# Kernel optimization log

Measured on AMD Instinct MI355X. Metric: run time of the kernel, lower is better.

## Reference

```python
import jax, jax.numpy as jnp
import numpy as np

B, L, G, H = 16384, 4096, 30000, 256
LN_EPS = 1e-5


def setup_inputs() -> dict:
    key = jax.random.key(0)
    k0, k1, k2, k3 = jax.random.split(key, 4)
    x = jax.random.uniform(k0, (B, L), dtype=jnp.float32)          # cell x gene expression
    gene_idx = jax.random.randint(k1, (L,), 0, G)                   # irregular gene indices
    emb = jax.random.normal(k2, (G, H), dtype=jnp.float32) * 0.005  # gene embedding table
    W1 = jax.random.normal(k3, (H, H), dtype=jnp.float32) * (1.0 / np.sqrt(H))
    b1 = jnp.zeros((H,), dtype=jnp.float32)
    gamma = jnp.ones((H,), dtype=jnp.float32)
    beta = jnp.zeros((H,), dtype=jnp.float32)
    return {"x": x, "emb": emb, "W1": W1, "b1": b1, "gamma": gamma,
            "beta": beta, "gene_idx": gene_idx}


def reference(x, emb, W1, b1, gamma, beta, gene_idx):
    # OmicsEmbedder: gather gene embeddings, then weighted aggregation per cell
    feat = emb[gene_idx]                     # [L, H]  F.embedding gather
    h = x @ feat                             # [B, H]  torch.sparse.mm(x, feat)
    # extra_linear: Linear -> ReLU -> Dropout(eval: identity) -> LayerNorm
    h = jax.nn.relu(h @ W1 + b1)             # [B, H]
    mu = jnp.mean(h, axis=-1, keepdims=True)
    var = jnp.mean(jnp.square(h - mu), axis=-1, keepdims=True)
    return gamma * (h - mu) * jax.lax.rsqrt(var + LN_EPS) + beta
```

## Files before the change

### kernel.cpp

```cpp
#include <hip/hip_runtime.h>
#include <stdint.h>

#define B_DIM 16384
#define L_DIM 4096
#define H_DIM 256
#define LN_EPS 1e-5f

typedef unsigned short u16;
typedef __attribute__((ext_vector_type(4))) float f32x4;
typedef __attribute__((ext_vector_type(8))) short short8;

__device__ __forceinline__ u16 f2bf(float f) {
  union { float f; uint32_t u; } v; v.f = f;
  uint32_t u = v.u;
  u += 0x7FFFu + ((u >> 16) & 1u);
  return (u16)(u >> 16);
}

__device__ __forceinline__ short8 cvt8(const float4& u, const float4& v) {
  short8 o;
  o[0] = (short)f2bf(u.x); o[1] = (short)f2bf(u.y);
  o[2] = (short)f2bf(u.z); o[3] = (short)f2bf(u.w);
  o[4] = (short)f2bf(v.x); o[5] = (short)f2bf(v.y);
  o[6] = (short)f2bf(v.z); o[7] = (short)f2bf(v.w);
  return o;
}

__device__ __forceinline__ void gload_lds16(const void* g, void* l) {
  __builtin_amdgcn_global_load_lds((const __attribute__((address_space(1))) void*)g,
                                   (__attribute__((address_space(3))) void*)l, 16, 0, 0);
}

__global__ __launch_bounds__(256) void prep_frag(const float* __restrict__ src,
                                                 const int* __restrict__ idx,
                                                 u16* __restrict__ dst) {
  const int t = threadIdx.x;
  const int l = t & 63;
  const int w = t >> 6;
  const int frag = blockIdx.x * 4 + w;
  const int kstep = frag >> 4;
  const int nt = frag & 15;
  const int n = nt * 16 + (l & 15);
  const int kbase = kstep * 32 + (l >> 4) * 8;
  short8 v;
#pragma unroll
  for (int j = 0; j < 8; ++j) {
    const int k = kbase + j;
    const int g = idx ? idx[k] : k;
    v[j] = (short)f2bf(src[(size_t)g * H_DIM + n]);
  }
  *reinterpret_cast<short8*>(dst + ((size_t)frag * 64 + l) * 8) = v;
}

__global__ __launch_bounds__(256, 2) void fused(const float* __restrict__ x,
                                                const u16* __restrict__ fragB,
                                                const u16* __restrict__ fragW,
                                                const float* __restrict__ b1,
                                                const float* __restrict__ gmm,
                                                const float* __restrict__ bta,
                                                float* __restrict__ out) {
  __shared__ __align__(16) char pool[73728];
  const int t = threadIdx.x;
  const int l = t & 63;
  const int wv = t >> 6;
  const int m0 = blockIdx.x * 32;
  char* const Ab = pool + 65536;

  const int sr = t >> 3;
  const int sc = t & 7;
  const float* xsrc = x + (size_t)(m0 + sr) * L_DIM + sc * 8;
  const int awoff = sr * 128 + ((sc ^ (sr & 7)) << 4);

  float4 aP0 = *(const float4*)(xsrc);
  float4 aP1 = *(const float4*)(xsrc + 4);
#pragma unroll
  for (int i = 0; i < 8; ++i) {
    const int j = wv * 8 + i;
    gload_lds16(fragB + (size_t)((j >> 4) * 16 + (j & 15)) * 512 + l * 8,
                pool + j * 1024);
  }
  float4 aQ0 = *(const float4*)(xsrc + 64);
  float4 aQ1 = *(const float4*)(xsrc + 68);
  asm volatile("s_waitcnt vmcnt(0)" ::: "memory");
  *(short8*)(Ab + awoff) = cvt8(aP0, aP1);
  asm volatile("s_waitcnt lgkmcnt(0)" ::: "memory");
  __builtin_amdgcn_s_barrier();

  f32x4 acc[2][4] = {};

  auto stage = [&](int S, const float4& WR0, const float4& WR1,
                   float4& LD0, float4& LD1) {
    asm volatile("s_waitcnt vmcnt(0)" ::: "memory");
    __builtin_amdgcn_s_barrier();
    __builtin_amdgcn_sched_barrier(0);
    if (S < 63) {
      const u16* srcB = fragB + (size_t)(2 * (S + 1)) * 16 * 512;
      char* dstB = pool + ((S + 1) & 1) * 32768;
#pragma unroll
      for (int i = 0; i < 8; ++i) {
        const int j = wv * 8 + i;
        gload_lds16(srcB + (size_t)((j >> 4) * 16 + (j & 15)) * 512 + l * 8,
                    dstB + j * 1024);
      }
    }
    __builtin_amdgcn_sched_barrier(0);
    if (S < 63)
      *(short8*)(Ab + ((S + 1) & 1) * 4096 + awoff) = cvt8(WR0, WR1);
    if (S < 62) {
      const float* xn = xsrc + (S + 2) * 64;
      LD0 = *(const float4*)(xn);
      LD1 = *(const float4*)(xn + 4);
    }
    __builtin_amdgcn_sched_barrier(0);
    const char* bB = pool + (S & 1) * 32768;
    const char* bA = Ab + (S & 1) * 4096;
#pragma unroll
    for (int ks = 0; ks < 2; ++ks) {
      short8 af[2];
#pragma unroll
      for (int mi = 0; mi < 2; ++mi)
        af[mi] = *(const short8*)(bA + (mi * 16 + (l & 15)) * 128 +
                                  (((ks * 4 + (l >> 4)) ^ (l & 7)) << 4));
#pragma unroll
      for (int ntl = 0; ntl < 4; ++ntl) {
        const short8 bfv = *(const short8*)(bB + (ks * 16 + wv * 4 + ntl) * 1024 + l * 16);
#pragma unroll
        for (int mi = 0; mi < 2; ++mi)
          acc[mi][ntl] = __builtin_amdgcn_mfma_f32_16x16x32_bf16(af[mi], bfv, acc[mi][ntl], 0, 0, 0);
      }
    }
    asm volatile("s_waitcnt lgkmcnt(0)" ::: "memory");
    __builtin_amdgcn_s_barrier();
  };

  for (int sp = 0; sp < 32; ++sp) {
    stage(sp * 2,     aQ0, aQ1, aP0, aP1);
    stage(sp * 2 + 1, aP0, aP1, aQ0, aQ1);
  }

#pragma unroll
  for (int i = 0; i < 4; ++i) {
    const int j = wv * 4 + i;
    gload_lds16(fragW + (size_t)j * 512 + l * 8, pool + 16384 + j * 1024);
  }
#pragma unroll
  for (int mi = 0; mi < 2; ++mi)
#pragma unroll
    for (int rr = 0; rr < 4; ++rr) {
      const int row = mi * 16 + (l >> 4) * 4 + rr;
#pragma unroll
      for (int ntl = 0; ntl < 4; ++ntl) {
        const int col = wv * 64 + ntl * 16 + (l & 15);
        const int ls = (col >> 3) ^ (row & 15);
        *(u16*)(pool + row * 512 + ls * 16 + (col & 7) * 2) = f2bf(acc[mi][ntl][rr]);
      }
    }
  asm volatile("s_waitcnt lgkmcnt(0)" ::: "memory");
  __builtin_amdgcn_s_barrier();

  f32x4 acc2[2][4] = {};
  for (int kt = 0; kt < 8; ++kt) {
    asm volatile("s_waitcnt vmcnt(0)" ::: "memory");
    __builtin_amdgcn_s_barrier();
    __builtin_amdgcn_sched_barrier(0);
    if (kt < 7) {
      const u16* srcW = fragW + (size_t)(kt + 1) * 16 * 512;
      char* dstW = pool + 16384 + ((kt + 1) & 1) * 16384;
#pragma unroll
      for (int i = 0; i < 4; ++i) {
        const int j = wv * 4 + i;
        gload_lds16(srcW + (size_t)j * 512 + l * 8, dstW + j * 1024);
      }
    }
    __builtin_amdgcn_sched_barrier(0);
    const char* bW = pool + 16384 + (kt & 1) * 16384;
    short8 af[2];
#pragma unroll
    for (int mi = 0; mi < 2; ++mi) {
      const int row = mi * 16 + (l & 15);
      af[mi] = *(const short8*)(pool + row * 512 +
                                (((kt * 4 + (l >> 4)) ^ (row & 15)) << 4));
    }
#pragma unroll
    for (int ntl = 0; ntl < 4; ++ntl) {
      const short8 bfv = *(const short8*)(bW + (wv * 4 + ntl) * 1024 + l * 16);
#pragma unroll
      for (int mi = 0; mi < 2; ++mi)
        acc2[mi][ntl] = __builtin_amdgcn_mfma_f32_16x16x32_bf16(af[mi], bfv, acc2[mi][ntl], 0, 0, 0);
    }
    asm volatile("s_waitcnt lgkmcnt(0)" ::: "memory");
    __builtin_amdgcn_s_barrier();
  }

  float bv[4], gg[4], bb[4];
#pragma unroll
  for (int ntl = 0; ntl < 4; ++ntl) {
    const int col = wv * 64 + ntl * 16 + (l & 15);
    bv[ntl] = b1[col]; gg[ntl] = gmm[col]; bb[ntl] = bta[col];
  }
  float* lnred = (float*)(pool + 49152);
#pragma unroll
  for (int mi = 0; mi < 2; ++mi)
#pragma unroll
    for (int rr = 0; rr < 4; ++rr) {
      float s = 0.f, q = 0.f;
#pragma unroll
      for (int ntl = 0; ntl < 4; ++ntl) {
        const float v = fmaxf(acc2[mi][ntl][rr] + bv[ntl], 0.f);
        acc2[mi][ntl][rr] = v; s += v; q += v * v;
      }
#pragma unroll
      for (int m = 1; m < 16; m <<= 1) { s += __shfl_xor(s, m); q += __shfl_xor(q, m); }
      if ((l & 15) == 0) {
        const int row = mi * 16 + (l >> 4) * 4 + rr;
        lnred[(wv * 32 + row) * 2 + 0] = s;
        lnred[(wv * 32 + row) * 2 + 1] = q;
      }
    }
  __syncthreads();
#pragma unroll
  for (int mi = 0; mi < 2; ++mi)
#pragma unroll
    for (int rr = 0; rr < 4; ++rr) {
      const int row = mi * 16 + (l >> 4) * 4 + rr;
      float S = 0.f, Q = 0.f;
#pragma unroll
      for (int w2 = 0; w2 < 4; ++w2) {
        S += lnred[(w2 * 32 + row) * 2 + 0];
        Q += lnred[(w2 * 32 + row) * 2 + 1];
      }
      const float mu = S * (1.0f / 256.0f);
      const float rstd = rsqrtf(Q * (1.0f / 256.0f) - mu * mu + LN_EPS);
      float* op = out + (size_t)(m0 + row) * H_DIM;
#pragma unroll
      for (int ntl = 0; ntl < 4; ++ntl) {
        const int col = wv * 64 + ntl * 16 + (l & 15);
        op[col] = gg[ntl] * (acc2[mi][ntl][rr] - mu) * rstd + bb[ntl];
      }
    }
}

extern "C" void kernel_launch(void* const* d_in, const int* in_sizes, int n_in,
                              void* d_out, int out_size, void* d_ws, size_t ws_size,
                              hipStream_t stream) {
  const float* x    = (const float*)d_in[0];
  const float* emb  = (const float*)d_in[1];
  const float* W1   = (const float*)d_in[2];
  const float* b1   = (const float*)d_in[3];
  const float* gmm  = (const float*)d_in[4];
  const float* bta  = (const float*)d_in[5];
  const int*   gidx = (const int*)d_in[6];
  float* out = (float*)d_out;

  char* ws = (char*)d_ws;
  u16* fragB = (u16*)ws;
  u16* fragW = (u16*)(ws + (size_t)H_DIM * L_DIM * 2);

  prep_frag<<<512, 256, 0, stream>>>(emb, gidx, fragB);
  prep_frag<<<32, 256, 0, stream>>>(W1, nullptr, fragW);
  fused<<<512, 256, 0, stream>>>(x, fragB, fragW, b1, gmm, bta, out);
}
```

Before: 108.9 us.

## Stream x tiles directly to LDS and load B fragments into registers

The main loop now copies fp32 x tiles straight from global memory into a swizzled, double-buffered LDS region with async global-to-LDS loads, and converts them to bf16 at fragment-read time. B fragments are no longer staged through LDS: each wave loads its own pre-packed fragments into registers, double-buffered across stages. This removes the register round trip and per-thread convert/store for x and the LDS traffic for B. In exchange it doubles the LDS bytes read for A, adds conversion work inside the MFMA loop, and raises register pressure under launch bounds of 2 blocks.

```diff
diff --git a/kernel.cpp b/kernel.cpp
--- a/kernel.cpp
+++ b/kernel.cpp
@@ -5,6 +5,7 @@
 #define L_DIM 4096
 #define H_DIM 256
 #define LN_EPS 1e-5f
+#define PERM4(r) ((((r) & 7) << 1) | (((r) >> 3) & 1))
 
 typedef unsigned short u16;
 typedef __attribute__((ext_vector_type(4))) float f32x4;
@@ -59,83 +60,75 @@
                                                 const float* __restrict__ gmm,
                                                 const float* __restrict__ bta,
                                                 float* __restrict__ out) {
-  __shared__ __align__(16) char pool[73728];
+  __shared__ __align__(16) char pool[81920];
   const int t = threadIdx.x;
   const int l = t & 63;
   const int wv = t >> 6;
   const int m0 = blockIdx.x * 32;
+  const float* xbase = x + (size_t)m0 * L_DIM;
   char* const Ab = pool + 65536;
 
-  const int sr = t >> 3;
-  const int sc = t & 7;
-  const float* xsrc = x + (size_t)(m0 + sr) * L_DIM + sc * 8;
-  const int awoff = sr * 128 + ((sc ^ (sr & 7)) << 4);
-
-  float4 aP0 = *(const float4*)(xsrc);
-  float4 aP1 = *(const float4*)(xsrc + 4);
-#pragma unroll
-  for (int i = 0; i < 8; ++i) {
-    const int j = wv * 8 + i;
-    gload_lds16(fragB + (size_t)((j >> 4) * 16 + (j & 15)) * 512 + l * 8,
-                pool + j * 1024);
-  }
-  float4 aQ0 = *(const float4*)(xsrc + 64);
-  float4 aQ1 = *(const float4*)(xsrc + 68);
-  asm volatile("s_waitcnt vmcnt(0)" ::: "memory");
-  *(short8*)(Ab + awoff) = cvt8(aP0, aP1);
-  asm volatile("s_waitcnt lgkmcnt(0)" ::: "memory");
-  __builtin_amdgcn_s_barrier();
-
   f32x4 acc[2][4] = {};
-
-  auto stage = [&](int S, const float4& WR0, const float4& WR1,
-                   float4& LD0, float4& LD1) {
+  short8 bP[8], bQ[8];
+
+#pragma unroll
+  for (int i = 0; i < 2; ++i) {
+    const int R = (wv * 2 + i) * 4 + (l >> 4);
+    const int c16 = (l & 15) ^ PERM4(R);
+    gload_lds16(xbase + (size_t)R * L_DIM + c16 * 4, Ab + (wv * 2 + i) * 1024);
+  }
+#pragma unroll
+  for (int f = 0; f < 8; ++f) {
+    const int frag = (f >> 2) * 16 + wv * 4 + (f & 3);
+    bP[f] = *(const short8*)(fragB + (size_t)frag * 512 + l * 8);
+  }
+
+  auto stage = [&](int S, short8 (&cur)[8], short8 (&nxt)[8]) {
     asm volatile("s_waitcnt vmcnt(0)" ::: "memory");
     __builtin_amdgcn_s_barrier();
     __builtin_amdgcn_sched_barrier(0);
     if (S < 63) {
-      const u16* srcB = fragB + (size_t)(2 * (S + 1)) * 16 * 512;
-      char* dstB = pool + ((S + 1) & 1) * 32768;
-#pragma unroll
-      for (int i = 0; i < 8; ++i) {
-        const int j = wv * 8 + i;
-        gload_lds16(srcB + (size_t)((j >> 4) * 16 + (j & 15)) * 512 + l * 8,
-                    dstB + j * 1024);
-      }
-    }
-    __builtin_amdgcn_sched_barrier(0);
-    if (S < 63)
-      *(short8*)(Ab + ((S + 1) & 1) * 4096 + awoff) = cvt8(WR0, WR1);
-    if (S < 62) {
-      const float* xn = xsrc + (S + 2) * 64;
-      LD0 = *(const float4*)(xn);
-      LD1 = *(const float4*)(xn + 4);
-    }
-    __builtin_amdgcn_sched_barrier(0);
-    const char* bB = pool + (S & 1) * 32768;
-    const char* bA = Ab + (S & 1) * 4096;
+#pragma unroll
+      for (int i = 0; i < 2; ++i) {
+        const int R = (wv * 2 + i) * 4 + (l >> 4);
+        const int c16 = (l & 15) ^ PERM4(R);
+        gload_lds16(xbase + (size_t)R * L_DIM + (S + 1) * 64 + c16 * 4,
+                    Ab + ((S + 1) & 1) * 8192 + (wv * 2 + i) * 1024);
+      }
+#pragma unroll
+      for (int f = 0; f < 8; ++f) {
+        const int frag = (2 * (S + 1) + (f >> 2)) * 16 + wv * 4 + (f & 3);
+        nxt[f] = *(const short8*)(fragB + (size_t)frag * 512 + l * 8);
+      }
+    }
+    __builtin_amdgcn_sched_barrier(0);
+    const char* bA = Ab + (S & 1) * 8192;
 #pragma unroll
     for (int ks = 0; ks < 2; ++ks) {
       short8 af[2];
 #pragma unroll
-      for (int mi = 0; mi < 2; ++mi)
-        af[mi] = *(const short8*)(bA + (mi * 16 + (l & 15)) * 128 +
-                                  (((ks * 4 + (l >> 4)) ^ (l & 7)) << 4));
-#pragma unroll
-      for (int ntl = 0; ntl < 4; ++ntl) {
-        const short8 bfv = *(const short8*)(bB + (ks * 16 + wv * 4 + ntl) * 1024 + l * 16);
+      for (int mi = 0; mi < 2; ++mi) {
+        const int row = mi * 16 + (l & 15);
+        const int p4 = PERM4(row);
+        const int gs = ks * 8 + (l >> 4) * 2;
+        const float4 a0 = *(const float4*)(bA + row * 256 + ((gs ^ p4) * 16));
+        const float4 a1 = *(const float4*)(bA + row * 256 + (((gs + 1) ^ p4) * 16));
+        af[mi] = cvt8(a0, a1);
+      }
+#pragma unroll
+      for (int ntl = 0; ntl < 4; ++ntl)
 #pragma unroll
         for (int mi = 0; mi < 2; ++mi)
-          acc[mi][ntl] = __builtin_amdgcn_mfma_f32_16x16x32_bf16(af[mi], bfv, acc[mi][ntl], 0, 0, 0);
-      }
+          acc[mi][ntl] = __builtin_amdgcn_mfma_f32_16x16x32_bf16(
+              af[mi], cur[ks * 4 + ntl], acc[mi][ntl], 0, 0, 0);
     }
     asm volatile("s_waitcnt lgkmcnt(0)" ::: "memory");
     __builtin_amdgcn_s_barrier();
   };
 
   for (int sp = 0; sp < 32; ++sp) {
-    stage(sp * 2,     aQ0, aQ1, aP0, aP1);
-    stage(sp * 2 + 1, aP0, aP1, aQ0, aQ1);
+    stage(sp * 2,     bP, bQ);
+    stage(sp * 2 + 1, bQ, bP);
   }
 
 #pragma unroll
```

Result: faster. 106.1 us (-2.5%).
